# Kernel optimization log

Hardware: AMD Instinct MI355X
Metric: run time of the kernel (lower is better)

## Reference

```python
import jax, jax.numpy as jnp
import numpy as np

NUM_HEADS = 16
NUM_KV_HEADS = 4
HEAD_DIM = 128
LAYER_IDX = 5
MASK_VALUE = -65504.0  # torch.finfo(torch.float16).min


def setup_inputs() -> dict:
    key = jax.random.key(0)
    ks = jax.random.split(key, 7)
    B, S, H = 2, 2048, 2048
    hidden_states = jax.random.normal(ks[0], (B, S, H), dtype=jnp.float32)
    k = jax.random.normal(ks[1], (B, NUM_KV_HEADS, S, HEAD_DIM), dtype=jnp.float32)
    v = jax.random.normal(ks[2], (B, NUM_KV_HEADS, S, HEAD_DIM), dtype=jnp.float32)
    std = 0.02
    w_q = jax.random.normal(ks[3], (H, H), dtype=jnp.float32) * std
    b_q = jnp.zeros((H,), dtype=jnp.float32)
    w_proj = jax.random.normal(ks[4], (H, H), dtype=jnp.float32) * (std / np.sqrt(2 * 24))
    b_proj = jnp.zeros((H,), dtype=jnp.float32)
    return {"hidden_states": hidden_states, "key": k, "value": v,
            "w_q": w_q, "b_q": b_q, "w_proj": w_proj, "b_proj": b_proj}


def reference(hidden_states, key, value, w_q, b_q, w_proj, b_proj):
    B, S, H = hidden_states.shape
    G = NUM_HEADS // NUM_KV_HEADS  # query heads per kv head
    dtype = hidden_states.dtype

    # query projection -> [B, kv_heads, group, S, head_dim]
    q = hidden_states @ w_q.T + b_q
    q = q.reshape(B, S, NUM_KV_HEADS, G, HEAD_DIM).transpose(0, 2, 3, 1, 4)

    # bigcode-style fp32 softmax with layer-wise unscale
    unscale = float(LAYER_IDX + 1)  # scale_attention_softmax_in_fp32 and upcast
    scale_factor = (1.0 / unscale) * (HEAD_DIM ** -0.5)  # scale_attn_weights

    # scores: [B, kv_heads, group, S_q, S_k]
    scores = jnp.einsum('bkgsd,bktd->bkgst', q, key) * scale_factor

    causal = jnp.tril(jnp.ones((S, S), dtype=bool))  # [S_q, S_k]
    scores = jnp.where(causal, scores, jnp.asarray(MASK_VALUE, dtype=scores.dtype))

    probs = jax.nn.softmax((scores * unscale).astype(jnp.float32), axis=-1).astype(dtype)

    out = jnp.einsum('bkgst,bktd->bkgsd', probs, value)
    out = out.transpose(0, 3, 1, 2, 4).reshape(B, S, H)
    out = out @ w_proj.T + b_proj
    return out
```

## Files before the change

kernel.cpp:

```cpp
#include <hip/hip_runtime.h>
#include <math.h>


#define RSQ128 0.08838834764831845
#define LOG2E  1.4426950408889634
#define RS2L   ((float)(RSQ128 * LOG2E))
#define MASK2  (-567000.0f)

typedef __attribute__((ext_vector_type(8))) short short8;
typedef __attribute__((ext_vector_type(4))) float f32x4;
typedef __attribute__((ext_vector_type(16))) float f32x16;

static __device__ __forceinline__ unsigned short f2bf(float x) {
    union { float f; unsigned u; } v; v.f = x;
    unsigned r = v.u + 0x7FFFu + ((v.u >> 16) & 1u);
    return (unsigned short)(r >> 16);
}

static __device__ __forceinline__ unsigned pack_bf16(float lo, float hi) {
#if __has_builtin(__builtin_amdgcn_cvt_pk_bf16_f32)
    return __builtin_bit_cast(unsigned, __builtin_amdgcn_cvt_pk_bf16_f32(lo, hi));
#else
    return (unsigned)f2bf(lo) | ((unsigned)f2bf(hi) << 16);
#endif
}

static __device__ __forceinline__ float fexp2(float x) {
#if __has_builtin(__builtin_amdgcn_exp2f)
    return __builtin_amdgcn_exp2f(x);
#else
    return exp2f(x);
#endif
}

static __device__ __forceinline__ void gl_lds16(const void* g, void* l) {
    __builtin_amdgcn_global_load_lds(
        (const __attribute__((address_space(1))) void*)g,
        (__attribute__((address_space(3))) void*)l, 16, 0, 0);
}

__global__ void cvt_bf16(const float* __restrict__ in, unsigned short* __restrict__ out) {
    const int i = (blockIdx.x * 256 + threadIdx.x) * 8;
    const float4 a = *(const float4*)(in + i);
    const float4 b = *(const float4*)(in + i + 4);
    short8 o;
    o[0] = (short)f2bf(a.x); o[1] = (short)f2bf(a.y);
    o[2] = (short)f2bf(a.z); o[3] = (short)f2bf(a.w);
    o[4] = (short)f2bf(b.x); o[5] = (short)f2bf(b.y);
    o[6] = (short)f2bf(b.z); o[7] = (short)f2bf(b.w);
    *(short8*)(out + i) = o;
}

__global__ void kprep_bf16(const float* __restrict__ K, unsigned short* __restrict__ Kpk) {
    const int t = blockIdx.x, bkh = blockIdx.y, tid = threadIdx.x;
    const float* src = K + ((size_t)bkh * 2048 + t * 32) * 128;
    unsigned short* dst = Kpk + ((size_t)bkh * 64 + t) * 4096;
#pragma unroll
    for (int p = 0; p < 2; ++p) {
        const int g = p * 256 + tid;
        const int ch = g >> 5, key = g & 31;
        const float4 a = *(const float4*)(src + key * 128 + ch * 8);
        const float4 b = *(const float4*)(src + key * 128 + ch * 8 + 4);
        short8 o;
        o[0] = (short)f2bf(a.x); o[1] = (short)f2bf(a.y);
        o[2] = (short)f2bf(a.z); o[3] = (short)f2bf(a.w);
        o[4] = (short)f2bf(b.x); o[5] = (short)f2bf(b.y);
        o[6] = (short)f2bf(b.z); o[7] = (short)f2bf(b.w);
        *(short8*)(dst + ch * 256 + key * 8) = o;
    }
}

__global__ void vprep_bf16(const float* __restrict__ V, unsigned short* __restrict__ Vpk) {
    __shared__ float Ts[32][132];
    const int t = blockIdx.x, bkh = blockIdx.y, tid = threadIdx.x;
    const float* src = V + ((size_t)bkh * 2048 + t * 32) * 128;
    unsigned short* dst = Vpk + ((size_t)bkh * 64 + t) * 4096;
#pragma unroll
    for (int p = 0; p < 4; ++p) {
        const int g = p * 256 + tid;
        const int key = g >> 5, cq = g & 31;
        const float4 v = *(const float4*)(src + key * 128 + cq * 4);
        *(float4*)&Ts[key][cq * 4] = v;
    }
    __syncthreads();
#pragma unroll
    for (int p = 0; p < 2; ++p) {
        const int g = p * 256 + tid;
        const int kc = g >> 7, d = g & 127;
        short8 o;
#pragma unroll
        for (int j = 0; j < 8; ++j) o[j] = (short)f2bf(Ts[kc * 8 + j][d]);
        *(short8*)(dst + kc * 1024 + d * 8) = o;
    }
}

template <bool BF16OUT>
__global__ __launch_bounds__(256, 2) void gemm_nt_mfma(
    const unsigned short* __restrict__ A,
    const unsigned short* __restrict__ W,
    const float* __restrict__ bias,
    void* __restrict__ Cout, int M, int N, int K, float oscale)
{
    __shared__ __align__(16) unsigned short As[2][4096];
    __shared__ __align__(16) unsigned short Ws[2][4096];
    const int tid = threadIdx.x, lane = tid & 63, w = tid >> 6;
    const int wm = w & 1, wn = w >> 1;
    const int m0 = blockIdx.y * 128, n0 = blockIdx.x * 128;
    const int r0 = tid >> 2, c0 = tid & 3;

    const unsigned short* Ag = A + (size_t)(m0 + r0) * K + c0 * 8;
    const unsigned short* Wg = W + (size_t)(n0 + r0) * K + c0 * 8;

    f32x4 acc[4][4];
#pragma unroll
    for (int i = 0; i < 4; ++i)
#pragma unroll
        for (int j = 0; j < 4; ++j) acc[i][j] = (f32x4){0.f, 0.f, 0.f, 0.f};

    const int lm = lane & 15, lk = (lane >> 4) * 8;

    gl_lds16(Ag,                  As[0] + tid * 8);
    gl_lds16(Ag + (size_t)64 * K, As[0] + (tid + 256) * 8);
    gl_lds16(Wg,                  Ws[0] + tid * 8);
    gl_lds16(Wg + (size_t)64 * K, Ws[0] + (tid + 256) * 8);

    int buf = 0;
    for (int k0 = 0; k0 < K; k0 += 32) {
        __syncthreads();
        const int kn = k0 + 32;
        if (kn < K) {
            unsigned short* Ad = As[buf ^ 1];
            unsigned short* Wd = Ws[buf ^ 1];
            gl_lds16(Ag + kn,                  Ad + tid * 8);
            gl_lds16(Ag + (size_t)64 * K + kn, Ad + (tid + 256) * 8);
            gl_lds16(Wg + kn,                  Wd + tid * 8);
            gl_lds16(Wg + (size_t)64 * K + kn, Wd + (tid + 256) * 8);
        }

        short8 a[4], b[4];
#pragma unroll
        for (int i = 0; i < 4; ++i)
            a[i] = *(const short8*)&As[buf][(64 * wm + 16 * i + lm) * 32 + lk];
#pragma unroll
        for (int j = 0; j < 4; ++j)
            b[j] = *(const short8*)&Ws[buf][(64 * wn + 16 * j + lm) * 32 + lk];
#pragma unroll
        for (int i = 0; i < 4; ++i)
#pragma unroll
            for (int j = 0; j < 4; ++j)
                acc[i][j] = __builtin_amdgcn_mfma_f32_16x16x32_bf16(a[i], b[j], acc[i][j], 0, 0, 0);
        buf ^= 1;
    }

    float bv[4];
#pragma unroll
    for (int j = 0; j < 4; ++j) bv[j] = bias[n0 + 64 * wn + 16 * j + lm];
#pragma unroll
    for (int i = 0; i < 4; ++i)
#pragma unroll
        for (int reg = 0; reg < 4; ++reg) {
            const int row = m0 + 64 * wm + 16 * i + 4 * (lane >> 4) + reg;
#pragma unroll
            for (int j = 0; j < 4; ++j) {
                const int col = n0 + 64 * wn + 16 * j + lm;
                const float v = (acc[i][j][reg] + bv[j]) * oscale;
                if (BF16OUT) ((unsigned short*)Cout)[(size_t)row * N + col] = f2bf(v);
                else         ((float*)Cout)[(size_t)row * N + col] = v;
            }
        }
}

__global__ __launch_bounds__(256, 4) void attn_mfma6(
    const unsigned short* __restrict__ Q,
    const unsigned short* __restrict__ Kpk,
    const unsigned short* __restrict__ Vpk,
    unsigned short* __restrict__ O)
{
    __shared__ __align__(16) unsigned short Ks[2][4096];
    __shared__ __align__(16) unsigned short Vs[2][4096];
    __shared__ float Msm[2][64], Lsm[2][64];

    const int tid = threadIdx.x, lane = tid & 63, w = tid >> 6;
    const int qhalf = w & 1, pz = w >> 1;
    const int h2 = lane >> 5, ln = lane & 31;

    const int bid = blockIdx.x;
    const int jj = bid >> 5;
    const int aa = jj & 7, bb = jj >> 3;
    const int qb = 8 * bb + ((bb & 1) ? (7 - aa) : aa);
    const int bh = bid & 31;
    const int s0 = qb * 64;
    const int b = bh >> 4, h = bh & 15, kh = h >> 2;

    const unsigned short* Kbase = Kpk + (size_t)(b * 4 + kh) * 64 * 4096;
    const unsigned short* Vbase = Vpk + (size_t)(b * 4 + kh) * 64 * 4096;

    const unsigned short* stsrc = (pz == 0 ? Kbase : Vbase) + (size_t)qhalf * 4096 + lane * 8;
    unsigned short* stdst = (pz == 0 ? Ks[qhalf] : Vs[qhalf]);

    const int qg = s0 + 32 * qhalf + ln;
    const unsigned short* Qp = Q + (size_t)(b * 2048 + qg) * 2048 + h * 128 + h2 * 8;
    short8 Qreg[8];
#pragma unroll
    for (int ks = 0; ks < 8; ++ks) Qreg[ks] = *(const short8*)(Qp + ks * 16);

    f32x16 Ot[4];
#pragma unroll
    for (int mt = 0; mt < 4; ++mt)
#pragma unroll
        for (int r = 0; r < 16; ++r) Ot[mt][r] = 0.f;
    float m_ = -INFINITY, l_ = 0.f;

    const int wq_hi = s0 + 32 * qhalf + 31;
    const int myofs = 32 * pz;

    for (int j = 0; j <= qb; ++j) {
        __syncthreads();
        {
            const unsigned short* sp = stsrc + (size_t)j * 8192;
#pragma unroll
            for (int i = 0; i < 8; ++i)
                gl_lds16(sp + i * 512, stdst + i * 512);
        }
        __syncthreads();

        const int t0 = 64 * j + myofs;
        if (t0 <= wq_hi) {
            const unsigned short* KsA = Ks[pz] + h2 * 256 + ln * 8;
            const unsigned short* VsA = Vs[pz] + h2 * 1024 + ln * 8;

            f32x16 St;
#pragma unroll
            for (int r = 0; r < 16; ++r) St[r] = 0.f;
#pragma unroll
            for (int ks = 0; ks < 8; ++ks) {
                const short8 a = *(const short8*)(KsA + ks * 512);
                St = __builtin_amdgcn_mfma_f32_32x32x16_bf16(a, Qreg[ks], St, 0, 0, 0);
            }

            float mx = -INFINITY;
            if (t0 + 31 <= s0 + 32 * qhalf) {
#pragma unroll
                for (int r = 0; r < 16; ++r) mx = fmaxf(mx, St[r]);
            } else {
#pragma unroll
                for (int r = 0; r < 16; ++r) {
                    const int key = t0 + (r & 3) + 8 * (r >> 2) + 4 * h2;
                    const float v = (key <= qg) ? St[r] : MASK2;
                    St[r] = v;
                    mx = fmaxf(mx, v);
                }
            }
            mx = fmaxf(mx, __shfl_xor(mx, 32));
            const float mn = fmaxf(m_, mx);
            float alpha = 1.f;
            if (__any(mx > m_)) {
                alpha = fexp2(m_ - mn);
#pragma unroll
                for (int mt = 0; mt < 4; ++mt)
#pragma unroll
                    for (int r = 0; r < 16; ++r) Ot[mt][r] *= alpha;
            }
            m_ = mn;

            float s_loc = 0.f;
            unsigned Pp[8];
#pragma unroll
            for (int p = 0; p < 8; ++p) {
                const float p0 = fexp2(St[2 * p] - mn);
                const float p1 = fexp2(St[2 * p + 1] - mn);
                s_loc += p0 + p1;
                Pp[p] = pack_bf16(p0, p1);
            }
            s_loc += __shfl_xor(s_loc, 32);
            l_ = l_ * alpha + s_loc;

#pragma unroll
            for (int ks4 = 0; ks4 < 2; ++ks4) {
                const unsigned pa = Pp[4 * ks4 + 0], pb = Pp[4 * ks4 + 1];
                const unsigned pc = Pp[4 * ks4 + 2], pd = Pp[4 * ks4 + 3];
                const unsigned x0 = (unsigned)__shfl_xor((int)(h2 ? pa : pc), 32);
                const unsigned x1 = (unsigned)__shfl_xor((int)(h2 ? pb : pd), 32);
                union { unsigned u[4]; short8 s8; } fr;
                fr.u[0] = h2 ? x0 : pa;
                fr.u[1] = h2 ? x1 : pb;
                fr.u[2] = h2 ? pc : x0;
                fr.u[3] = h2 ? pd : x1;
#pragma unroll
                for (int mt = 0; mt < 4; ++mt) {
                    const short8 a = *(const short8*)(VsA + ks4 * 2048 + mt * 256);
                    Ot[mt] = __builtin_amdgcn_mfma_f32_32x32x16_bf16(a, fr.s8, Ot[mt], 0, 0, 0);
                }
            }
        }
    }

    __syncthreads();
    if (pz == 1) {
        float* dst = qhalf ? (float*)Vs : (float*)Ks;
#pragma unroll
        for (int mt = 0; mt < 4; ++mt)
#pragma unroll
            for (int g = 0; g < 4; ++g) {
                float4 v4;
                v4.x = Ot[mt][4 * g + 0]; v4.y = Ot[mt][4 * g + 1];
                v4.z = Ot[mt][4 * g + 2]; v4.w = Ot[mt][4 * g + 3];
                *(float4*)&dst[lane * 64 + (((mt * 4 + g + lane) & 15) * 4)] = v4;
            }
        Msm[qhalf][lane] = m_;
        Lsm[qhalf][lane] = l_;
    }
    __syncthreads();
    if (pz == 0) {
        const float m1 = Msm[qhalf][lane];
        const float l1 = Lsm[qhalf][lane];
        const float* src = qhalf ? (const float*)Vs : (const float*)Ks;
        const float mM = fmaxf(m_, m1);
        const float a0 = fexp2(m_ - mM);
        const float a1 = fexp2(m1 - mM);
        l_ = l_ * a0 + l1 * a1;
#pragma unroll
        for (int mt = 0; mt < 4; ++mt)
#pragma unroll
            for (int g = 0; g < 4; ++g) {
                const float4 v4 = *(const float4*)&src[lane * 64 + (((mt * 4 + g + lane) & 15) * 4)];
                Ot[mt][4 * g + 0] = Ot[mt][4 * g + 0] * a0 + v4.x * a1;
                Ot[mt][4 * g + 1] = Ot[mt][4 * g + 1] * a0 + v4.y * a1;
                Ot[mt][4 * g + 2] = Ot[mt][4 * g + 2] * a0 + v4.z * a1;
                Ot[mt][4 * g + 3] = Ot[mt][4 * g + 3] * a0 + v4.w * a1;
            }
    }
    __syncthreads();

    if (pz == 0) {
        unsigned short* Es = (unsigned short*)Ks + qhalf * 4096;
        const float inv = 1.0f / l_;
#pragma unroll
        for (int mt = 0; mt < 4; ++mt)
#pragma unroll
            for (int g = 0; g < 4; ++g) {
                uint2 pk;
                pk.x = pack_bf16(Ot[mt][4 * g + 0] * inv, Ot[mt][4 * g + 1] * inv);
                pk.y = pack_bf16(Ot[mt][4 * g + 2] * inv, Ot[mt][4 * g + 3] * inv);
                const int chunk = (4 * mt + g) ^ (ln & 15);
                *(uint2*)&Es[ln * 128 + chunk * 8 + 4 * h2] = pk;
            }
    }
    __syncthreads();
    if (pz == 0) {
        unsigned short* Es = (unsigned short*)Ks + qhalf * 4096;
#pragma unroll
        for (int pp = 0; pp < 8; ++pp) {
            const int f = pp * 64 + lane;
            const int q = f >> 4, c = f & 15;
            const short8 v = *(const short8*)&Es[q * 128 + ((c ^ (q & 15)) * 8)];
            *(short8*)(O + (size_t)(b * 2048 + s0 + 32 * qhalf + q) * 2048 + h * 128 + c * 8) = v;
        }
    }
}

extern "C" void kernel_launch(void* const* d_in, const int* in_sizes, int n_in,
                              void* d_out, int out_size, void* d_ws, size_t ws_size,
                              hipStream_t stream) {
    const float* hs = (const float*)d_in[0];
    const float* k  = (const float*)d_in[1];
    const float* v  = (const float*)d_in[2];
    const float* wq = (const float*)d_in[3];
    const float* bq = (const float*)d_in[4];
    const float* wp = (const float*)d_in[5];
    const float* bp = (const float*)d_in[6];
    float* out = (float*)d_out;

    unsigned short* hsb  = (unsigned short*)d_ws;
    unsigned short* wqb  = hsb  + 8388608;
    unsigned short* kpk  = wqb  + 4194304;
    unsigned short* vpk  = kpk  + 2097152;
    unsigned short* qbuf = vpk  + 2097152;
    unsigned short* abuf = qbuf + 8388608;
    unsigned short* wpb  = hsb;

    cvt_bf16<<<4096, 256, 0, stream>>>(hs, hsb);
    cvt_bf16<<<2048, 256, 0, stream>>>(wq, wqb);
    kprep_bf16<<<dim3(64, 8), 256, 0, stream>>>(k, kpk);
    vprep_bf16<<<dim3(64, 8), 256, 0, stream>>>(v, vpk);

    dim3 gG(16, 32);
    gemm_nt_mfma<true><<<gG, 256, 0, stream>>>(hsb, wqb, bq, qbuf, 4096, 2048, 2048, RS2L);
    cvt_bf16<<<2048, 256, 0, stream>>>(wp, wpb);
    attn_mfma6<<<1024, 256, 0, stream>>>(qbuf, kpk, vpk, abuf);
    gemm_nt_mfma<false><<<gG, 256, 0, stream>>>(abuf, wpb, bp, out, 4096, 2048, 2048, 1.0f);
}
```

Baseline: 313.4 us.

## Split GEMM K dimension across two warp groups within a block

```diff
diff --git a/kernel.cpp b/kernel.cpp
--- a/kernel.cpp
+++ b/kernel.cpp
@@ -95,21 +95,28 @@
 }
 
 template <bool BF16OUT>
-__global__ __launch_bounds__(256, 2) void gemm_nt_mfma(
+__global__ __launch_bounds__(512, 2) void gemm_nt_sk(
     const unsigned short* __restrict__ A,
     const unsigned short* __restrict__ W,
     const float* __restrict__ bias,
     void* __restrict__ Cout, int M, int N, int K, float oscale)
 {
-    __shared__ __align__(16) unsigned short As[2][4096];
-    __shared__ __align__(16) unsigned short Ws[2][4096];
-    const int tid = threadIdx.x, lane = tid & 63, w = tid >> 6;
-    const int wm = w & 1, wn = w >> 1;
+    __shared__ __align__(16) unsigned short SMEM[32768];
+    unsigned short* Asb = SMEM;
+    unsigned short* Wsb = SMEM + 16384;
+
+    const int tid = threadIdx.x;
+    const int g = tid >> 8;
+    const int t2 = tid & 255;
+    const int lane = tid & 63;
+    const int wq = (tid >> 6) & 3;
+    const int wm = wq & 1, wn = wq >> 1;
     const int m0 = blockIdx.y * 128, n0 = blockIdx.x * 128;
-    const int r0 = tid >> 2, c0 = tid & 3;
-
-    const unsigned short* Ag = A + (size_t)(m0 + r0) * K + c0 * 8;
-    const unsigned short* Wg = W + (size_t)(n0 + r0) * K + c0 * 8;
+    const int r0 = t2 >> 2, c0 = t2 & 3;
+    const int Kh = K >> 1;
+
+    const unsigned short* Ag = A + (size_t)(m0 + r0) * K + g * Kh + c0 * 8;
+    const unsigned short* Wg = W + (size_t)(n0 + r0) * K + g * Kh + c0 * 8;
 
     f32x4 acc[4][4];
 #pragma unroll
@@ -118,32 +125,36 @@
         for (int j = 0; j < 4; ++j) acc[i][j] = (f32x4){0.f, 0.f, 0.f, 0.f};
 
     const int lm = lane & 15, lk = (lane >> 4) * 8;
-
-    gl_lds16(Ag,                  As[0] + tid * 8);
-    gl_lds16(Ag + (size_t)64 * K, As[0] + (tid + 256) * 8);
-    gl_lds16(Wg,                  Ws[0] + tid * 8);
-    gl_lds16(Wg + (size_t)64 * K, Ws[0] + (tid + 256) * 8);
+    unsigned short* As0 = Asb + g * 8192;
+    unsigned short* Ws0 = Wsb + g * 8192;
+
+    gl_lds16(Ag,                  As0 + t2 * 8);
+    gl_lds16(Ag + (size_t)64 * K, As0 + (t2 + 256) * 8);
+    gl_lds16(Wg,                  Ws0 + t2 * 8);
+    gl_lds16(Wg + (size_t)64 * K, Ws0 + (t2 + 256) * 8);
 
     int buf = 0;
-    for (int k0 = 0; k0 < K; k0 += 32) {
+    for (int k0 = 0; k0 < Kh; k0 += 32) {
         __syncthreads();
         const int kn = k0 + 32;
-        if (kn < K) {
-            unsigned short* Ad = As[buf ^ 1];
-            unsigned short* Wd = Ws[buf ^ 1];
-            gl_lds16(Ag + kn,                  Ad + tid * 8);
-            gl_lds16(Ag + (size_t)64 * K + kn, Ad + (tid + 256) * 8);
-            gl_lds16(Wg + kn,                  Wd + tid * 8);
-            gl_lds16(Wg + (size_t)64 * K + kn, Wd + (tid + 256) * 8);
+        if (kn < Kh) {
+            unsigned short* Ad = As0 + (buf ^ 1) * 4096;
+            unsigned short* Wd = Ws0 + (buf ^ 1) * 4096;
+            gl_lds16(Ag + kn,                  Ad + t2 * 8);
+            gl_lds16(Ag + (size_t)64 * K + kn, Ad + (t2 + 256) * 8);
+            gl_lds16(Wg + kn,                  Wd + t2 * 8);
+            gl_lds16(Wg + (size_t)64 * K + kn, Wd + (t2 + 256) * 8);
         }
 
+        const unsigned short* Ar = As0 + buf * 4096;
+        const unsigned short* Wr = Ws0 + buf * 4096;
         short8 a[4], b[4];
 #pragma unroll
         for (int i = 0; i < 4; ++i)
-            a[i] = *(const short8*)&As[buf][(64 * wm + 16 * i + lm) * 32 + lk];
+            a[i] = *(const short8*)&Ar[(64 * wm + 16 * i + lm) * 32 + lk];
 #pragma unroll
         for (int j = 0; j < 4; ++j)
-            b[j] = *(const short8*)&Ws[buf][(64 * wn + 16 * j + lm) * 32 + lk];
+            b[j] = *(const short8*)&Wr[(64 * wn + 16 * j + lm) * 32 + lk];
 #pragma unroll
         for (int i = 0; i < 4; ++i)
 #pragma unroll
@@ -152,22 +163,40 @@
         buf ^= 1;
     }
 
-    float bv[4];
-#pragma unroll
-    for (int j = 0; j < 4; ++j) bv[j] = bias[n0 + 64 * wn + 16 * j + lm];
-#pragma unroll
-    for (int i = 0; i < 4; ++i)
-#pragma unroll
-        for (int reg = 0; reg < 4; ++reg) {
-            const int row = m0 + 64 * wm + 16 * i + 4 * (lane >> 4) + reg;
+    float* MRG = (float*)SMEM;
+    __syncthreads();
+    if (g == 1) {
+#pragma unroll
+        for (int i = 0; i < 4; ++i)
 #pragma unroll
             for (int j = 0; j < 4; ++j) {
-                const int col = n0 + 64 * wn + 16 * j + lm;
-                const float v = (acc[i][j][reg] + bv[j]) * oscale;
-                if (BF16OUT) ((unsigned short*)Cout)[(size_t)row * N + col] = f2bf(v);
-                else         ((float*)Cout)[(size_t)row * N + col] = v;
-            }
-        }
+                float4 v4;
+                v4.x = acc[i][j][0]; v4.y = acc[i][j][1];
+                v4.z = acc[i][j][2]; v4.w = acc[i][j][3];
+                *(float4*)&MRG[((i * 4 + j) * 256 + wq * 64 + lane) * 4] = v4;
+            }
+    }
+    __syncthreads();
+    if (g == 0) {
+        float bv[4];
+#pragma unroll
+        for (int j = 0; j < 4; ++j) bv[j] = bias[n0 + 64 * wn + 16 * j + lm];
+#pragma unroll
+        for (int i = 0; i < 4; ++i)
+#pragma unroll
+            for (int j = 0; j < 4; ++j) {
+                const float4 v4 = *(const float4*)&MRG[((i * 4 + j) * 256 + wq * 64 + lane) * 4];
+                const float s[4] = {v4.x, v4.y, v4.z, v4.w};
+#pragma unroll
+                for (int reg = 0; reg < 4; ++reg) {
+                    const int row = m0 + 64 * wm + 16 * i + 4 * (lane >> 4) + reg;
+                    const int col = n0 + 64 * wn + 16 * j + lm;
+                    const float v = (acc[i][j][reg] + s[reg] + bv[j]) * oscale;
+                    if (BF16OUT) ((unsigned short*)Cout)[(size_t)row * N + col] = f2bf(v);
+                    else         ((float*)Cout)[(size_t)row * N + col] = v;
+                }
+            }
+    }
 }
 
 __global__ __launch_bounds__(256, 4) void attn_mfma6(
@@ -385,8 +414,8 @@
     vprep_bf16<<<dim3(64, 8), 256, 0, stream>>>(v, vpk);
 
     dim3 gG(16, 32);
-    gemm_nt_mfma<true><<<gG, 256, 0, stream>>>(hsb, wqb, bq, qbuf, 4096, 2048, 2048, RS2L);
+    gemm_nt_sk<true><<<gG, 512, 0, stream>>>(hsb, wqb, bq, qbuf, 4096, 2048, 2048, RS2L);
     cvt_bf16<<<2048, 256, 0, stream>>>(wp, wpb);
     attn_mfma6<<<1024, 256, 0, stream>>>(qbuf, kpk, vpk, abuf);
-    gemm_nt_mfma<false><<<gG, 256, 0, stream>>>(abuf, wpb, bp, out, 4096, 2048, 2048, 1.0f);
-}
+    gemm_nt_sk<false><<<gG, 512, 0, stream>>>(abuf, wpb, bp, out, 4096, 2048, 2048, 1.0f);
+}
```

Result: faster. 305.3 us (-2.6%).
